# Kernel optimization log

Hardware: AMD Instinct MI355X
Metric: run time of the kernel (lower is better)

The kernel has to match this reference:

```python
import jax, jax.numpy as jnp
import numpy as np

B, S, D_IN, D_OUT, H = 2, 2048, 1024, 1024, 16
HD = D_OUT // H  # 64


def setup_inputs() -> dict:
    key = jax.random.key(0)
    ks = jax.random.split(key, 6)
    s = 0.02
    return {
        "x": jax.random.normal(ks[0], (B, S, D_IN), dtype=jnp.float32),
        "W_q": jax.random.normal(ks[1], (D_IN, D_OUT), dtype=jnp.float32) * s,
        "W_k": jax.random.normal(ks[2], (D_IN, D_OUT), dtype=jnp.float32) * s,
        "W_v": jax.random.normal(ks[3], (D_IN, D_OUT), dtype=jnp.float32) * s,
        "W_o": jax.random.normal(ks[4], (D_OUT, D_OUT), dtype=jnp.float32) * s,
        "b_o": jax.random.normal(ks[5], (D_OUT,), dtype=jnp.float32) * s,
    }


def reference(x, W_q, W_k, W_v, W_o, b_o):
    b, n, _ = x.shape
    # project and split heads: [b, h, n, hd]
    q = (x @ W_q).reshape(b, n, H, HD).transpose(0, 2, 1, 3)
    k = (x @ W_k).reshape(b, n, H, HD).transpose(0, 2, 1, 3)
    v = (x @ W_v).reshape(b, n, H, HD).transpose(0, 2, 1, 3)
    scores = jnp.einsum("bhqd,bhkd->bhqk", q, k) / jnp.sqrt(jnp.float32(HD))
    causal = jnp.tril(jnp.ones((n, n), dtype=bool))
    scores = jnp.where(causal, scores, -jnp.inf)
    attn = jax.nn.softmax(scores, axis=-1)  # dropout p=0.0 -> identity
    ctx = jnp.einsum("bhqk,bhkd->bhqd", attn, v)
    ctx = ctx.transpose(0, 2, 1, 3).reshape(b, n, D_OUT)
    return ctx @ W_o + b_o
```

## Files before the change

### kernel.cpp

```cpp
#include <hip/hip_runtime.h>

#define B_    2
#define S_    2048
#define DIN   1024
#define DOUT  1024
#define H_    16
#define HD_   64
#define M_    (B_ * S_)

typedef __bf16 bf16x8 __attribute__((ext_vector_type(8)));
typedef float  f32x4  __attribute__((ext_vector_type(4)));

__device__ __forceinline__ f32x4 MFMA(bf16x8 a, bf16x8 b, f32x4 c) {
    return __builtin_amdgcn_mfma_f32_16x16x32_bf16(a, b, c, 0, 0, 0);
}

__device__ __forceinline__ unsigned short f2b(float f) {
    union { float f; unsigned int u; } v; v.f = f;
    unsigned int u = v.u;
    return (unsigned short)((u + 0x7fffu + ((u >> 16) & 1u)) >> 16);
}

__device__ __forceinline__ unsigned pack2(float a, float b) {
    union { __bf16 h[2]; unsigned u; } cv;
    cv.h[0] = (__bf16)a; cv.h[1] = (__bf16)b;
    return cv.u;
}

#define GLDS(gp, lp) __builtin_amdgcn_global_load_lds( \
    (const __attribute__((address_space(1))) void*)(gp), \
    (__attribute__((address_space(3))) void*)(lp), 16, 0, 0)

#define QSCALE 0.1803368801111204f

__global__ __launch_bounds__(256) void k_cvt_all(const float* __restrict__ x,
                                                 const float* __restrict__ Wq,
                                                 const float* __restrict__ Wk,
                                                 const float* __restrict__ Wv,
                                                 const float* __restrict__ Wo,
                                                 unsigned short* __restrict__ xb,
                                                 unsigned short* __restrict__ WqkvT,
                                                 unsigned short* __restrict__ WoT) {
    __shared__ float tile[32][33];
    int bid = blockIdx.x;
    if (bid < 4096) {
        int i = (bid * 256 + threadIdx.x) * 4;
        float4 v = *reinterpret_cast<const float4*>(x + i);
        ushort4 o;
        o.x = f2b(v.x); o.y = f2b(v.y); o.z = f2b(v.z); o.w = f2b(v.w);
        *reinterpret_cast<ushort4*>(xb + i) = o;
        return;
    }
    int wb = bid - 4096;
    int w = wb >> 10;
    int t = wb & 1023;
    const float* src = (w == 0) ? Wq : (w == 1) ? Wk : (w == 2) ? Wv : Wo;
    unsigned short* dst = (w < 3) ? WqkvT + (size_t)w * 1024 * DIN : WoT;
    int n0 = (t & 31) * 32, k0 = (t >> 5) * 32;
    int tx = threadIdx.x & 31, ty = threadIdx.x >> 5;
    for (int i = 0; i < 4; i++)
        tile[ty + i * 8][tx] = src[(size_t)(k0 + ty + i * 8) * DOUT + n0 + tx];
    __syncthreads();
    for (int i = 0; i < 4; i++)
        dst[(size_t)(n0 + ty + i * 8) * DIN + k0 + tx] = f2b(tile[tx][ty + i * 8]);
}

__global__ __launch_bounds__(256) void k_trV(const unsigned short* __restrict__ V,
                                             unsigned short* __restrict__ Vt) {
    __shared__ unsigned short tile[64][72];
    int st = blockIdx.x, bh = blockIdx.y;
    int b = bh >> 4, h = bh & 15;
    int t = threadIdx.x;
    int r = t >> 2, c = (t & 3) << 4;
    const unsigned short* src = V + (size_t)(b * S_ + st * 64 + r) * DOUT + h * HD_ + c;
    *reinterpret_cast<int4*>(&tile[r][c])     = *reinterpret_cast<const int4*>(src);
    *reinterpret_cast<int4*>(&tile[r][c + 8]) = *reinterpret_cast<const int4*>(src + 8);
    __syncthreads();
    unsigned short o[16];
    for (int j = 0; j < 16; j++) o[j] = tile[c + j][r];
    unsigned short* dst = Vt + (size_t)(bh * 64 + r) * S_ + st * 64 + c;
    *reinterpret_cast<int4*>(dst)     = *reinterpret_cast<int4*>(&o[0]);
    *reinterpret_cast<int4*>(dst + 8) = *reinterpret_cast<int4*>(&o[8]);
}

template <int OUT_MODE>
__global__ __launch_bounds__(256) void k_gemm(const unsigned short* __restrict__ A,
                                              const unsigned short* __restrict__ Bt,
                                              unsigned short* __restrict__ Cq,
                                              unsigned short* __restrict__ Ck,
                                              unsigned short* __restrict__ Cv,
                                              float* __restrict__ Cf,
                                              const float* __restrict__ bias,
                                              int M, int N, int K, int nbx) {
    __shared__ __align__(16) unsigned short As[128 * 64];
    __shared__ __align__(16) unsigned short Bs[128 * 64];

    int nwg = gridDim.x;
    int chunkw = nwg >> 3;
    int bid = blockIdx.x;
    int nid = (bid & 7) * chunkw + (bid >> 3);
    int by = nid / nbx, bx = nid - by * nbx;
    int m0 = by * 128, n0 = bx * 128;

    int tid = threadIdx.x;
    int wid = tid >> 6, lane = tid & 63;
    int wm = wid >> 1, wn = wid & 1;
    int lr = lane & 15, lg = lane >> 4;

    f32x4 acc[4][4] = {};

    int srow = lane >> 3;
    int scol = ((lane & 7) ^ srow) * 8;
    int rsw  = lr & 7;

    for (int k0 = 0; k0 < K; k0 += 64) {
#pragma unroll
        for (int c = 0; c < 4; c++) {
            int chunk = wid * 4 + c;
            int row = chunk * 8 + srow;
            GLDS(A  + (size_t)(m0 + row) * K + k0 + scol, (char*)As + chunk * 1024);
            GLDS(Bt + (size_t)(n0 + row) * K + k0 + scol, (char*)Bs + chunk * 1024);
        }
        __syncthreads();

#pragma unroll
        for (int kk = 0; kk < 2; kk++) {
            bf16x8 af[4], bf[4];
#pragma unroll
            for (int mi = 0; mi < 4; mi++)
                af[mi] = *reinterpret_cast<const bf16x8*>(
                    &As[(wm * 64 + mi * 16 + lr) * 64 + (((kk * 4 + lg) ^ rsw) * 8)]);
#pragma unroll
            for (int ni = 0; ni < 4; ni++)
                bf[ni] = *reinterpret_cast<const bf16x8*>(
                    &Bs[(wn * 64 + ni * 16 + lr) * 64 + (((kk * 4 + lg) ^ rsw) * 8)]);
#pragma unroll
            for (int mi = 0; mi < 4; mi++)
#pragma unroll
                for (int ni = 0; ni < 4; ni++)
                    acc[mi][ni] = MFMA(af[mi], bf[ni], acc[mi][ni]);
        }
        __syncthreads();
    }

    for (int mi = 0; mi < 4; mi++)
        for (int ni = 0; ni < 4; ni++)
            for (int i = 0; i < 4; i++) {
                int row = m0 + wm * 64 + mi * 16 + lg * 4 + i;
                int col = n0 + wn * 64 + ni * 16 + lr;
                float v = acc[mi][ni][i];
                if (OUT_MODE == 2) {
                    Cf[(size_t)row * N + col] = v + bias[col];
                } else {
                    if (col < 1024)       Cq[(size_t)row * 1024 + col] = f2b(v * QSCALE);
                    else if (col < 2048)  Ck[(size_t)row * 1024 + (col - 1024)] = f2b(v);
                    else                  Cv[(size_t)row * 1024 + (col - 2048)] = f2b(v);
                }
            }
}

__global__ __launch_bounds__(512, 4) void k_attn(const unsigned short* __restrict__ Q,
                                                 const unsigned short* __restrict__ Kg,
                                                 const unsigned short* __restrict__ Vt,
                                                 unsigned short* __restrict__ ctx) {
    int p = blockIdx.x;
    int bh = blockIdx.y;
    int b = bh >> 4, h = bh & 15;
    int tid = threadIdx.x, wid = tid >> 6, lane = tid & 63;
    int lr = lane & 15, lg = lane >> 4;
    int qtB = 31 - p;
    int qt = (wid < 4) ? qtB : p;
    int q0 = qt * 64 + (wid & 3) * 16;

    __shared__ __align__(16) unsigned short Ks[2][64 * 64];
    __shared__ __align__(16) unsigned short Vs[2][64 * 64];
    __shared__ __align__(16) unsigned p_lds32[8][16 * 32];
    unsigned* pl32 = p_lds32[wid];

    const unsigned short* Qp = Q  + (size_t)b * S_ * DOUT + (size_t)h * HD_;
    const unsigned short* Kp = Kg + (size_t)b * S_ * DOUT + (size_t)h * HD_;
    const unsigned short* Vp = Vt + (size_t)(b * H_ + h) * HD_ * S_;

    bf16x8 qf0 = *reinterpret_cast<const bf16x8*>(&Qp[(size_t)(q0 + lr) * DOUT + lg * 8]);
    bf16x8 qf1 = *reinterpret_cast<const bf16x8*>(&Qp[(size_t)(q0 + lr) * DOUT + 32 + lg * 8]);
    asm volatile("" : "+v"(qf0), "+v"(qf1));

    int srow = lane >> 3;
    int scol = ((lane & 7) ^ srow) * 8;

#define STAGE_KV(buf, t)                                                           \
    {                                                                              \
        int kv0_ = (t) * 64;                                                       \
        int krow = wid * 8 + srow;                                                 \
        GLDS(Kp + (size_t)(kv0_ + krow) * DOUT + scol,                             \
             (char*)&Ks[buf][0] + wid * 1024);                                     \
        GLDS(Vp + (size_t)krow * S_ + kv0_ + scol,                                 \
             (char*)&Vs[buf][0] + wid * 1024);                                     \
    }

    STAGE_KV(0, 0)

    f32x4 o[4] = {};
    float l = 0.f;

    int ntile = qtB + 1;
    int rxor = (lr & 7) << 4;
    int qg = q0 + lr;

    for (int t = 0; t < ntile; t++) {
        int cur = t & 1;
        if (t + 1 < ntile) {
            STAGE_KV(cur ^ 1, t + 1)
            asm volatile("s_waitcnt vmcnt(2)" ::: "memory");
        } else {
            asm volatile("s_waitcnt vmcnt(0)" ::: "memory");
        }
        __builtin_amdgcn_s_barrier();

        if (t <= qt) {
            const unsigned short* Kt = Ks[cur];
            const unsigned short* Vl = Vs[cur];
            int kv0 = t * 64;

            f32x4 s[4] = {};
            __builtin_amdgcn_s_setprio(1);
#pragma unroll
            for (int nf = 0; nf < 4; nf++)
#pragma unroll
                for (int kk = 0; kk < 2; kk++) {
                    bf16x8 kf = *reinterpret_cast<const bf16x8*>(
                        &Kt[(nf * 16 + lr) * 64 + (((kk * 64 + lg * 16) ^ rxor) >> 1)]);
                    s[nf] = MFMA(kf, kk ? qf1 : qf0, s[nf]);
                }
            __builtin_amdgcn_s_setprio(0);

            if (t == qt) {
#pragma unroll
                for (int nf = 0; nf < 4; nf++)
#pragma unroll
                    for (int i = 0; i < 4; i++)
                        if (kv0 + nf * 16 + lg * 4 + i > qg) s[nf][i] = -2000.0f;
            }

            f32x4 acc = {};
#pragma unroll
            for (int nf = 0; nf < 4; nf++) {
                f32x4 pv;
#pragma unroll
                for (int i = 0; i < 4; i++) pv[i] = exp2f(s[nf][i]);
                acc += pv;
                unsigned w0 = pack2(pv[0], pv[1]);
                unsigned w1 = pack2(pv[2], pv[3]);
                int unit = (nf * 2 + (lg >> 1)) ^ (lr & 7);
                uint2 wd; wd.x = w0; wd.y = w1;
                *reinterpret_cast<uint2*>(&pl32[lr * 32 + unit * 4 + (lg & 1) * 2]) = wd;
            }
            l += (acc[0] + acc[1]) + (acc[2] + acc[3]);

            bf16x8 pf[2];
#pragma unroll
            for (int kvb = 0; kvb < 2; kvb++)
                pf[kvb] = *reinterpret_cast<const bf16x8*>(
                    &pl32[lr * 32 + (((kvb * 4 + lg) ^ (lr & 7)) * 4)]);

            __builtin_amdgcn_s_setprio(1);
#pragma unroll
            for (int nd = 0; nd < 4; nd++)
#pragma unroll
                for (int kk = 0; kk < 2; kk++) {
                    bf16x8 vf = *reinterpret_cast<const bf16x8*>(
                        &Vl[(nd * 16 + lr) * 64 + (((kk * 64 + lg * 16) ^ rxor) >> 1)]);
                    o[nd] = MFMA(pf[kk], vf, o[nd]);
                }
            __builtin_amdgcn_s_setprio(0);
        }

        __builtin_amdgcn_s_barrier();
    }

    l += __shfl_xor(l, 16, 64);
    l += __shfl_xor(l, 32, 64);

#pragma unroll
    for (int i = 0; i < 4; i++) {
        float li = __shfl(l, lg * 4 + i, 16);
        float r = __builtin_amdgcn_rcpf(li);
#pragma unroll
        for (int nd = 0; nd < 4; nd++)
            ((__bf16*)ctx)[((size_t)b * S_ + q0 + lg * 4 + i) * DOUT + h * HD_ + nd * 16 + lr] =
                (__bf16)(o[nd][i] * r);
    }
#undef STAGE_KV
}

extern "C" void kernel_launch(void* const* d_in, const int* in_sizes, int n_in,
                              void* d_out, int out_size, void* d_ws, size_t ws_size,
                              hipStream_t stream) {
    const float* x  = (const float*)d_in[0];
    const float* Wq = (const float*)d_in[1];
    const float* Wk = (const float*)d_in[2];
    const float* Wv = (const float*)d_in[3];
    const float* Wo = (const float*)d_in[4];
    const float* bo = (const float*)d_in[5];
    float* out = (float*)d_out;
    char* ws = (char*)d_ws;
    const size_t MB = 1u << 20;

    unsigned short* xb    = (unsigned short*)(ws);
    unsigned short* Vtb   = (unsigned short*)(ws);
    unsigned short* WqkvT = (unsigned short*)(ws + 8 * MB);
    unsigned short* WoT   = (unsigned short*)(ws + 14 * MB);
    unsigned short* Qb    = (unsigned short*)(ws + 16 * MB);
    unsigned short* Kb    = (unsigned short*)(ws + 24 * MB);
    unsigned short* Vb    = (unsigned short*)(ws + 32 * MB);
    unsigned short* ctx   = Vb;

    (void)in_sizes; (void)n_in; (void)out_size; (void)ws_size;

    k_cvt_all<<<8192, 256, 0, stream>>>(x, Wq, Wk, Wv, Wo, xb, WqkvT, WoT);

    k_gemm<0><<<768, 256, 0, stream>>>(xb, WqkvT, Qb, Kb, Vb, nullptr, nullptr,
                                       M_, 3072, DIN, 24);

    dim3 gt(S_ / 64, B_ * H_);
    k_trV<<<gt, 256, 0, stream>>>(Vb, Vtb);

    dim3 ga(16, B_ * H_);
    k_attn<<<ga, 512, 0, stream>>>(Qb, Kb, Vtb, ctx);

    k_gemm<2><<<256, 256, 0, stream>>>(ctx, WoT, nullptr, nullptr, nullptr,
                                       out, bo, M_, DOUT, DOUT, 8);
}
```

Before: 120.8 us.

## Process two 16-row query slices per wave in attention, halving block size

Each attention wave now handles 32 query rows (two 16-row MFMA slices) instead of 16, so the block shrinks from 8 to 4 waves while covering the same two 64-row query tiles. Each K/V fragment read from LDS feeds two MFMAs, which halves LDS read traffic per FLOP, and each wave now issues two global-to-LDS loads per tile. The trade-off is doubled accumulator and score registers per wave and fewer waves per block for hiding latency.

After: 140.0 us. 15.9% more time.

```diff
diff --git a/kernel.cpp b/kernel.cpp
--- a/kernel.cpp
+++ b/kernel.cpp
@@ -159,7 +159,7 @@
             }
 }
 
-__global__ __launch_bounds__(512, 4) void k_attn(const unsigned short* __restrict__ Q,
+__global__ __launch_bounds__(256, 4) void k_attn(const unsigned short* __restrict__ Q,
                                                  const unsigned short* __restrict__ Kg,
                                                  const unsigned short* __restrict__ Vt,
                                                  unsigned short* __restrict__ ctx) {
@@ -169,21 +169,23 @@
     int tid = threadIdx.x, wid = tid >> 6, lane = tid & 63;
     int lr = lane & 15, lg = lane >> 4;
     int qtB = 31 - p;
-    int qt = (wid < 4) ? qtB : p;
-    int q0 = qt * 64 + (wid & 3) * 16;
+    int qt = (wid < 2) ? qtB : p;
+    int q0 = qt * 64 + (wid & 1) * 32;
 
     __shared__ __align__(16) unsigned short Ks[2][64 * 64];
     __shared__ __align__(16) unsigned short Vs[2][64 * 64];
-    __shared__ __align__(16) unsigned p_lds32[8][16 * 32];
+    __shared__ __align__(16) unsigned p_lds32[4][16 * 32];
     unsigned* pl32 = p_lds32[wid];
 
     const unsigned short* Qp = Q  + (size_t)b * S_ * DOUT + (size_t)h * HD_;
     const unsigned short* Kp = Kg + (size_t)b * S_ * DOUT + (size_t)h * HD_;
     const unsigned short* Vp = Vt + (size_t)(b * H_ + h) * HD_ * S_;
 
-    bf16x8 qf0 = *reinterpret_cast<const bf16x8*>(&Qp[(size_t)(q0 + lr) * DOUT + lg * 8]);
-    bf16x8 qf1 = *reinterpret_cast<const bf16x8*>(&Qp[(size_t)(q0 + lr) * DOUT + 32 + lg * 8]);
-    asm volatile("" : "+v"(qf0), "+v"(qf1));
+    bf16x8 qf0a = *reinterpret_cast<const bf16x8*>(&Qp[(size_t)(q0 + lr) * DOUT + lg * 8]);
+    bf16x8 qf0b = *reinterpret_cast<const bf16x8*>(&Qp[(size_t)(q0 + lr) * DOUT + 32 + lg * 8]);
+    bf16x8 qf1a = *reinterpret_cast<const bf16x8*>(&Qp[(size_t)(q0 + 16 + lr) * DOUT + lg * 8]);
+    bf16x8 qf1b = *reinterpret_cast<const bf16x8*>(&Qp[(size_t)(q0 + 16 + lr) * DOUT + 32 + lg * 8]);
+    asm volatile("" : "+v"(qf0a), "+v"(qf0b), "+v"(qf1a), "+v"(qf1b));
 
     int srow = lane >> 3;
     int scol = ((lane & 7) ^ srow) * 8;
@@ -191,27 +193,30 @@
 #define STAGE_KV(buf, t)                                                           \
     {                                                                              \
         int kv0_ = (t) * 64;                                                       \
-        int krow = wid * 8 + srow;                                                 \
-        GLDS(Kp + (size_t)(kv0_ + krow) * DOUT + scol,                             \
-             (char*)&Ks[buf][0] + wid * 1024);                                     \
-        GLDS(Vp + (size_t)krow * S_ + kv0_ + scol,                                 \
-             (char*)&Vs[buf][0] + wid * 1024);                                     \
+        for (int cc = 0; cc < 2; cc++) {                                           \
+            int ch = wid * 2 + cc;                                                 \
+            int krow = ch * 8 + srow;                                              \
+            GLDS(Kp + (size_t)(kv0_ + krow) * DOUT + scol,                         \
+                 (char*)&Ks[buf][0] + ch * 1024);                                  \
+            GLDS(Vp + (size_t)krow * S_ + kv0_ + scol,                             \
+                 (char*)&Vs[buf][0] + ch * 1024);                                  \
+        }                                                                          \
     }
 
     STAGE_KV(0, 0)
 
-    f32x4 o[4] = {};
-    float l = 0.f;
+    f32x4 o0[4] = {}, o1[4] = {};
+    float l0 = 0.f, l1 = 0.f;
 
     int ntile = qtB + 1;
     int rxor = (lr & 7) << 4;
-    int qg = q0 + lr;
+    int qg0 = q0 + lr, qg1 = q0 + 16 + lr;
 
     for (int t = 0; t < ntile; t++) {
         int cur = t & 1;
         if (t + 1 < ntile) {
             STAGE_KV(cur ^ 1, t + 1)
-            asm volatile("s_waitcnt vmcnt(2)" ::: "memory");
+            asm volatile("s_waitcnt vmcnt(4)" ::: "memory");
         } else {
             asm volatile("s_waitcnt vmcnt(0)" ::: "memory");
         }
@@ -222,7 +227,7 @@
             const unsigned short* Vl = Vs[cur];
             int kv0 = t * 64;
 
-            f32x4 s[4] = {};
+            f32x4 s0[4] = {}, s1[4] = {};
             __builtin_amdgcn_s_setprio(1);
 #pragma unroll
             for (int nf = 0; nf < 4; nf++)
@@ -230,7 +235,8 @@
                 for (int kk = 0; kk < 2; kk++) {
                     bf16x8 kf = *reinterpret_cast<const bf16x8*>(
                         &Kt[(nf * 16 + lr) * 64 + (((kk * 64 + lg * 16) ^ rxor) >> 1)]);
-                    s[nf] = MFMA(kf, kk ? qf1 : qf0, s[nf]);
+                    s0[nf] = MFMA(kf, kk ? qf0b : qf0a, s0[nf]);
+                    s1[nf] = MFMA(kf, kk ? qf1b : qf1a, s1[nf]);
                 }
             __builtin_amdgcn_s_setprio(0);
 
@@ -238,30 +244,50 @@
 #pragma unroll
                 for (int nf = 0; nf < 4; nf++)
 #pragma unroll
-                    for (int i = 0; i < 4; i++)
-                        if (kv0 + nf * 16 + lg * 4 + i > qg) s[nf][i] = -2000.0f;
+                    for (int i = 0; i < 4; i++) {
+                        int kv = kv0 + nf * 16 + lg * 4 + i;
+                        if (kv > qg0) s0[nf][i] = -2000.0f;
+                        if (kv > qg1) s1[nf][i] = -2000.0f;
+                    }
             }
 
-            f32x4 acc = {};
-#pragma unroll
-            for (int nf = 0; nf < 4; nf++) {
-                f32x4 pv;
-#pragma unroll
-                for (int i = 0; i < 4; i++) pv[i] = exp2f(s[nf][i]);
-                acc += pv;
-                unsigned w0 = pack2(pv[0], pv[1]);
-                unsigned w1 = pack2(pv[2], pv[3]);
-                int unit = (nf * 2 + (lg >> 1)) ^ (lr & 7);
-                uint2 wd; wd.x = w0; wd.y = w1;
-                *reinterpret_cast<uint2*>(&pl32[lr * 32 + unit * 4 + (lg & 1) * 2]) = wd;
+            bf16x8 pf0[2], pf1[2];
+            {
+                f32x4 acc = {};
+#pragma unroll
+                for (int nf = 0; nf < 4; nf++) {
+                    f32x4 pv;
+#pragma unroll
+                    for (int i = 0; i < 4; i++) pv[i] = exp2f(s0[nf][i]);
+                    acc += pv;
+                    int unit = (nf * 2 + (lg >> 1)) ^ (lr & 7);
+                    uint2 wd; wd.x = pack2(pv[0], pv[1]); wd.y = pack2(pv[2], pv[3]);
+                    *reinterpret_cast<uint2*>(&pl32[lr * 32 + unit * 4 + (lg & 1) * 2]) = wd;
+                }
+                l0 += (acc[0] + acc[1]) + (acc[2] + acc[3]);
+#pragma unroll
+                for (int kvb = 0; kvb < 2; kvb++)
+                    pf0[kvb] = *reinterpret_cast<const bf16x8*>(
+                        &pl32[lr * 32 + (((kvb * 4 + lg) ^ (lr & 7)) * 4)]);
             }
-            l += (acc[0] + acc[1]) + (acc[2] + acc[3]);
-
-            bf16x8 pf[2];
-#pragma unroll
-            for (int kvb = 0; kvb < 2; kvb++)
-                pf[kvb] = *reinterpret_cast<const bf16x8*>(
-                    &pl32[lr * 32 + (((kvb * 4 + lg) ^ (lr & 7)) * 4)]);
+            {
+                f32x4 acc = {};
+#pragma unroll
+                for (int nf = 0; nf < 4; nf++) {
+                    f32x4 pv;
+#pragma unroll
+                    for (int i = 0; i < 4; i++) pv[i] = exp2f(s1[nf][i]);
+                    acc += pv;
+                    int unit = (nf * 2 + (lg >> 1)) ^ (lr & 7);
+                    uint2 wd; wd.x = pack2(pv[0], pv[1]); wd.y = pack2(pv[2], pv[3]);
+                    *reinterpret_cast<uint2*>(&pl32[lr * 32 + unit * 4 + (lg & 1) * 2]) = wd;
+                }
+                l1 += (acc[0] + acc[1]) + (acc[2] + acc[3]);
+#pragma unroll
+                for (int kvb = 0; kvb < 2; kvb++)
+                    pf1[kvb] = *reinterpret_cast<const bf16x8*>(
+                        &pl32[lr * 32 + (((kvb * 4 + lg) ^ (lr & 7)) * 4)]);
+            }
 
             __builtin_amdgcn_s_setprio(1);
 #pragma unroll
@@ -270,7 +296,8 @@
                 for (int kk = 0; kk < 2; kk++) {
                     bf16x8 vf = *reinterpret_cast<const bf16x8*>(
                         &Vl[(nd * 16 + lr) * 64 + (((kk * 64 + lg * 16) ^ rxor) >> 1)]);
-                    o[nd] = MFMA(pf[kk], vf, o[nd]);
+                    o0[nd] = MFMA(pf0[kk], vf, o0[nd]);
+                    o1[nd] = MFMA(pf1[kk], vf, o1[nd]);
                 }
             __builtin_amdgcn_s_setprio(0);
         }
@@ -278,17 +305,24 @@
         __builtin_amdgcn_s_barrier();
     }
 
-    l += __shfl_xor(l, 16, 64);
-    l += __shfl_xor(l, 32, 64);
+    l0 += __shfl_xor(l0, 16, 64);
+    l0 += __shfl_xor(l0, 32, 64);
+    l1 += __shfl_xor(l1, 16, 64);
+    l1 += __shfl_xor(l1, 32, 64);
 
 #pragma unroll
     for (int i = 0; i < 4; i++) {
-        float li = __shfl(l, lg * 4 + i, 16);
-        float r = __builtin_amdgcn_rcpf(li);
-#pragma unroll
-        for (int nd = 0; nd < 4; nd++)
+        float li0 = __shfl(l0, lg * 4 + i, 16);
+        float li1 = __shfl(l1, lg * 4 + i, 16);
+        float r0 = __builtin_amdgcn_rcpf(li0);
+        float r1 = __builtin_amdgcn_rcpf(li1);
+#pragma unroll
+        for (int nd = 0; nd < 4; nd++) {
             ((__bf16*)ctx)[((size_t)b * S_ + q0 + lg * 4 + i) * DOUT + h * HD_ + nd * 16 + lr] =
-                (__bf16)(o[nd][i] * r);
+                (__bf16)(o0[nd][i] * r0);
+            ((__bf16*)ctx)[((size_t)b * S_ + q0 + 16 + lg * 4 + i) * DOUT + h * HD_ + nd * 16 + lr] =
+                (__bf16)(o1[nd][i] * r1);
+        }
     }
 #undef STAGE_KV
 }
@@ -326,7 +360,7 @@
     k_trV<<<gt, 256, 0, stream>>>(Vb, Vtb);
 
     dim3 ga(16, B_ * H_);
-    k_attn<<<ga, 512, 0, stream>>>(Qb, Kb, Vtb, ctx);
+    k_attn<<<ga, 256, 0, stream>>>(Qb, Kb, Vtb, ctx);
 
     k_gemm<2><<<256, 256, 0, stream>>>(ctx, WoT, nullptr, nullptr, nullptr,
                                        out, bo, M_, DOUT, DOUT, 8);
```

## Split long causal query tile across wave groups and shrink output GEMM tile

Applied to the files above, without the earlier changes.

The attention kernel previously had one wave group process the long query tile while the other sat idle after its short tile. Now the second group finishes its short tile, then takes the remaining KV tiles of the long tile, and the two partial outputs and row sums are merged through LDS at the end. Each group gets its own double-buffered K/V staging. Separately, the output projection GEMM is templated to a 64-row M tile with twice as many blocks, to give better occupancy on a grid that was smaller than the CU count. The cost is more LDS per attention block, an extra reduction step, and lower per-block data reuse in the GEMM.

New measurement: 112.8 us. -6.6%, faster.

```diff
diff --git a/kernel.cpp b/kernel.cpp
--- a/kernel.cpp
+++ b/kernel.cpp
@@ -83,7 +83,7 @@
     *reinterpret_cast<int4*>(dst + 8) = *reinterpret_cast<int4*>(&o[8]);
 }
 
-template <int OUT_MODE>
+template <int OUT_MODE, int BM>
 __global__ __launch_bounds__(256) void k_gemm(const unsigned short* __restrict__ A,
                                               const unsigned short* __restrict__ Bt,
                                               unsigned short* __restrict__ Cq,
@@ -92,7 +92,8 @@
                                               float* __restrict__ Cf,
                                               const float* __restrict__ bias,
                                               int M, int N, int K, int nbx) {
-    __shared__ __align__(16) unsigned short As[128 * 64];
+    constexpr int MI = BM / 32;
+    __shared__ __align__(16) unsigned short As[BM * 64];
     __shared__ __align__(16) unsigned short Bs[128 * 64];
 
     int nwg = gridDim.x;
@@ -100,14 +101,14 @@
     int bid = blockIdx.x;
     int nid = (bid & 7) * chunkw + (bid >> 3);
     int by = nid / nbx, bx = nid - by * nbx;
-    int m0 = by * 128, n0 = bx * 128;
+    int m0 = by * BM, n0 = bx * 128;
 
     int tid = threadIdx.x;
     int wid = tid >> 6, lane = tid & 63;
     int wm = wid >> 1, wn = wid & 1;
     int lr = lane & 15, lg = lane >> 4;
 
-    f32x4 acc[4][4] = {};
+    f32x4 acc[MI][4] = {};
 
     int srow = lane >> 3;
     int scol = ((lane & 7) ^ srow) * 8;
@@ -115,27 +116,32 @@
 
     for (int k0 = 0; k0 < K; k0 += 64) {
 #pragma unroll
+        for (int c = 0; c < MI; c++) {
+            int chunk = wid * MI + c;
+            int row = chunk * 8 + srow;
+            GLDS(A + (size_t)(m0 + row) * K + k0 + scol, (char*)As + chunk * 1024);
+        }
+#pragma unroll
         for (int c = 0; c < 4; c++) {
             int chunk = wid * 4 + c;
             int row = chunk * 8 + srow;
-            GLDS(A  + (size_t)(m0 + row) * K + k0 + scol, (char*)As + chunk * 1024);
             GLDS(Bt + (size_t)(n0 + row) * K + k0 + scol, (char*)Bs + chunk * 1024);
         }
         __syncthreads();
 
 #pragma unroll
         for (int kk = 0; kk < 2; kk++) {
-            bf16x8 af[4], bf[4];
-#pragma unroll
-            for (int mi = 0; mi < 4; mi++)
+            bf16x8 af[MI], bf[4];
+#pragma unroll
+            for (int mi = 0; mi < MI; mi++)
                 af[mi] = *reinterpret_cast<const bf16x8*>(
-                    &As[(wm * 64 + mi * 16 + lr) * 64 + (((kk * 4 + lg) ^ rsw) * 8)]);
+                    &As[(wm * (BM / 2) + mi * 16 + lr) * 64 + (((kk * 4 + lg) ^ rsw) * 8)]);
 #pragma unroll
             for (int ni = 0; ni < 4; ni++)
                 bf[ni] = *reinterpret_cast<const bf16x8*>(
                     &Bs[(wn * 64 + ni * 16 + lr) * 64 + (((kk * 4 + lg) ^ rsw) * 8)]);
 #pragma unroll
-            for (int mi = 0; mi < 4; mi++)
+            for (int mi = 0; mi < MI; mi++)
 #pragma unroll
                 for (int ni = 0; ni < 4; ni++)
                     acc[mi][ni] = MFMA(af[mi], bf[ni], acc[mi][ni]);
@@ -143,10 +149,10 @@
         __syncthreads();
     }
 
-    for (int mi = 0; mi < 4; mi++)
+    for (int mi = 0; mi < MI; mi++)
         for (int ni = 0; ni < 4; ni++)
             for (int i = 0; i < 4; i++) {
-                int row = m0 + wm * 64 + mi * 16 + lg * 4 + i;
+                int row = m0 + wm * (BM / 2) + mi * 16 + lg * 4 + i;
                 int col = n0 + wn * 64 + ni * 16 + lr;
                 float v = acc[mi][ni][i];
                 if (OUT_MODE == 2) {
@@ -159,6 +165,64 @@
             }
 }
 
+__device__ __forceinline__ void attn_unit(const unsigned short* __restrict__ Kt,
+                                          const unsigned short* __restrict__ Vl,
+                                          unsigned* __restrict__ pl32,
+                                          bf16x8 qf0, bf16x8 qf1,
+                                          f32x4 (&o)[4], float& l,
+                                          int qg, int kv0, bool diag,
+                                          int lr, int lg, int rxor) {
+    f32x4 s[4] = {};
+    __builtin_amdgcn_s_setprio(1);
+#pragma unroll
+    for (int nf = 0; nf < 4; nf++)
+#pragma unroll
+        for (int kk = 0; kk < 2; kk++) {
+            bf16x8 kf = *reinterpret_cast<const bf16x8*>(
+                &Kt[(nf * 16 + lr) * 64 + (((kk * 64 + lg * 16) ^ rxor) >> 1)]);
+            s[nf] = MFMA(kf, kk ? qf1 : qf0, s[nf]);
+        }
+    __builtin_amdgcn_s_setprio(0);
+
+    if (diag) {
+#pragma unroll
+        for (int nf = 0; nf < 4; nf++)
+#pragma unroll
+            for (int i = 0; i < 4; i++)
+                if (kv0 + nf * 16 + lg * 4 + i > qg) s[nf][i] = -2000.0f;
+    }
+
+    f32x4 acc = {};
+#pragma unroll
+    for (int nf = 0; nf < 4; nf++) {
+        f32x4 pv;
+#pragma unroll
+        for (int i = 0; i < 4; i++) pv[i] = exp2f(s[nf][i]);
+        acc += pv;
+        int unit = (nf * 2 + (lg >> 1)) ^ (lr & 7);
+        uint2 wd; wd.x = pack2(pv[0], pv[1]); wd.y = pack2(pv[2], pv[3]);
+        *reinterpret_cast<uint2*>(&pl32[lr * 32 + unit * 4 + (lg & 1) * 2]) = wd;
+    }
+    l += (acc[0] + acc[1]) + (acc[2] + acc[3]);
+
+    bf16x8 pf[2];
+#pragma unroll
+    for (int kvb = 0; kvb < 2; kvb++)
+        pf[kvb] = *reinterpret_cast<const bf16x8*>(
+            &pl32[lr * 32 + (((kvb * 4 + lg) ^ (lr & 7)) * 4)]);
+
+    __builtin_amdgcn_s_setprio(1);
+#pragma unroll
+    for (int nd = 0; nd < 4; nd++)
+#pragma unroll
+        for (int kk = 0; kk < 2; kk++) {
+            bf16x8 vf = *reinterpret_cast<const bf16x8*>(
+                &Vl[(nd * 16 + lr) * 64 + (((kk * 64 + lg * 16) ^ rxor) >> 1)]);
+            o[nd] = MFMA(pf[kk], vf, o[nd]);
+        }
+    __builtin_amdgcn_s_setprio(0);
+}
+
 __global__ __launch_bounds__(512, 4) void k_attn(const unsigned short* __restrict__ Q,
                                                  const unsigned short* __restrict__ Kg,
                                                  const unsigned short* __restrict__ Vt,
@@ -168,12 +232,13 @@
     int b = bh >> 4, h = bh & 15;
     int tid = threadIdx.x, wid = tid >> 6, lane = tid & 63;
     int lr = lane & 15, lg = lane >> 4;
+    int g = wid >> 2, wi = wid & 3;
     int qtB = 31 - p;
-    int qt = (wid < 4) ? qtB : p;
-    int q0 = qt * 64 + (wid & 3) * 16;
-
-    __shared__ __align__(16) unsigned short Ks[2][64 * 64];
-    __shared__ __align__(16) unsigned short Vs[2][64 * 64];
+
+    __shared__ __align__(16) unsigned short Ks1[2][64 * 64];
+    __shared__ __align__(16) unsigned short Vs1[2][64 * 64];
+    __shared__ __align__(16) unsigned short Ks2[2][64 * 64];
+    __shared__ __align__(16) unsigned short Vs2[2][64 * 64];
     __shared__ __align__(16) unsigned p_lds32[8][16 * 32];
     unsigned* pl32 = p_lds32[wid];
 
@@ -181,116 +246,124 @@
     const unsigned short* Kp = Kg + (size_t)b * S_ * DOUT + (size_t)h * HD_;
     const unsigned short* Vp = Vt + (size_t)(b * H_ + h) * HD_ * S_;
 
-    bf16x8 qf0 = *reinterpret_cast<const bf16x8*>(&Qp[(size_t)(q0 + lr) * DOUT + lg * 8]);
-    bf16x8 qf1 = *reinterpret_cast<const bf16x8*>(&Qp[(size_t)(q0 + lr) * DOUT + 32 + lg * 8]);
-    asm volatile("" : "+v"(qf0), "+v"(qf1));
+    int q0B = qtB * 64 + wi * 16;
+    int q0A = p * 64 + wi * 16;
+
+    bf16x8 qB0 = *reinterpret_cast<const bf16x8*>(&Qp[(size_t)(q0B + lr) * DOUT + lg * 8]);
+    bf16x8 qB1 = *reinterpret_cast<const bf16x8*>(&Qp[(size_t)(q0B + lr) * DOUT + 32 + lg * 8]);
+    bf16x8 qA0 = {}, qA1 = {};
+    if (g == 1) {
+        qA0 = *reinterpret_cast<const bf16x8*>(&Qp[(size_t)(q0A + lr) * DOUT + lg * 8]);
+        qA1 = *reinterpret_cast<const bf16x8*>(&Qp[(size_t)(q0A + lr) * DOUT + 32 + lg * 8]);
+    }
+    asm volatile("" : "+v"(qB0), "+v"(qB1));
 
     int srow = lane >> 3;
     int scol = ((lane & 7) ^ srow) * 8;
 
-#define STAGE_KV(buf, t)                                                           \
+#define STAGE(KsX, VsX, buf, t)                                                    \
     {                                                                              \
         int kv0_ = (t) * 64;                                                       \
-        int krow = wid * 8 + srow;                                                 \
-        GLDS(Kp + (size_t)(kv0_ + krow) * DOUT + scol,                             \
-             (char*)&Ks[buf][0] + wid * 1024);                                     \
-        GLDS(Vp + (size_t)krow * S_ + kv0_ + scol,                                 \
-             (char*)&Vs[buf][0] + wid * 1024);                                     \
-    }
-
-    STAGE_KV(0, 0)
-
-    f32x4 o[4] = {};
-    float l = 0.f;
-
-    int ntile = qtB + 1;
+        for (int cc = 0; cc < 2; cc++) {                                           \
+            int ch = wi * 2 + cc;                                                  \
+            int krow = ch * 8 + srow;                                              \
+            GLDS(Kp + (size_t)(kv0_ + krow) * DOUT + scol,                         \
+                 (char*)&KsX[buf][0] + ch * 1024);                                 \
+            GLDS(Vp + (size_t)krow * S_ + kv0_ + scol,                             \
+                 (char*)&VsX[buf][0] + ch * 1024);                                 \
+        }                                                                          \
+    }
+
+    if (g == 0) STAGE(Ks1, Vs1, 0, 0)
+    else        STAGE(Ks2, Vs2, 0, 0)
+
+    f32x4 oB[4] = {}, oA[4] = {};
+    float lB = 0.f, lA = 0.f;
     int rxor = (lr & 7) << 4;
-    int qg = q0 + lr;
-
-    for (int t = 0; t < ntile; t++) {
-        int cur = t & 1;
-        if (t + 1 < ntile) {
-            STAGE_KV(cur ^ 1, t + 1)
-            asm volatile("s_waitcnt vmcnt(2)" ::: "memory");
+    int qgB = q0B + lr, qgA = q0A + lr;
+
+    for (int u = 0; u <= 16; u++) {
+        if (g == 0) {
+            if (u < 15) {
+                STAGE(Ks1, Vs1, (u + 1) & 1, u + 1)
+                asm volatile("s_waitcnt vmcnt(4)" ::: "memory");
+            } else {
+                asm volatile("s_waitcnt vmcnt(0)" ::: "memory");
+            }
         } else {
-            asm volatile("s_waitcnt vmcnt(0)" ::: "memory");
+            if (u < 16) {
+                int nt = (u + 1 <= p) ? (u + 1) : (u + 16 - p);
+                STAGE(Ks2, Vs2, (u + 1) & 1, nt)
+                asm volatile("s_waitcnt vmcnt(4)" ::: "memory");
+            } else {
+                asm volatile("s_waitcnt vmcnt(0)" ::: "memory");
+            }
         }
         __builtin_amdgcn_s_barrier();
 
-        if (t <= qt) {
-            const unsigned short* Kt = Ks[cur];
-            const unsigned short* Vl = Vs[cur];
-            int kv0 = t * 64;
-
-            f32x4 s[4] = {};
-            __builtin_amdgcn_s_setprio(1);
-#pragma unroll
-            for (int nf = 0; nf < 4; nf++)
-#pragma unroll
-                for (int kk = 0; kk < 2; kk++) {
-                    bf16x8 kf = *reinterpret_cast<const bf16x8*>(
-                        &Kt[(nf * 16 + lr) * 64 + (((kk * 64 + lg * 16) ^ rxor) >> 1)]);
-                    s[nf] = MFMA(kf, kk ? qf1 : qf0, s[nf]);
-                }
-            __builtin_amdgcn_s_setprio(0);
-
-            if (t == qt) {
-#pragma unroll
-                for (int nf = 0; nf < 4; nf++)
-#pragma unroll
-                    for (int i = 0; i < 4; i++)
-                        if (kv0 + nf * 16 + lg * 4 + i > qg) s[nf][i] = -2000.0f;
+        if (g == 0) {
+            if (u <= 15)
+                attn_unit(Ks1[u & 1], Vs1[u & 1], pl32, qB0, qB1, oB, lB,
+                          qgB, u * 64, false, lr, lg, rxor);
+        } else {
+            if (u <= p)
+                attn_unit(Ks2[u & 1], Vs2[u & 1], pl32, qA0, qA1, oA, lA,
+                          qgA, u * 64, u == p, lr, lg, rxor);
+            else {
+                int t = u + 15 - p;
+                attn_unit(Ks2[u & 1], Vs2[u & 1], pl32, qB0, qB1, oB, lB,
+                          qgB, t * 64, t == qtB, lr, lg, rxor);
             }
-
-            f32x4 acc = {};
-#pragma unroll
-            for (int nf = 0; nf < 4; nf++) {
-                f32x4 pv;
-#pragma unroll
-                for (int i = 0; i < 4; i++) pv[i] = exp2f(s[nf][i]);
-                acc += pv;
-                unsigned w0 = pack2(pv[0], pv[1]);
-                unsigned w1 = pack2(pv[2], pv[3]);
-                int unit = (nf * 2 + (lg >> 1)) ^ (lr & 7);
-                uint2 wd; wd.x = w0; wd.y = w1;
-                *reinterpret_cast<uint2*>(&pl32[lr * 32 + unit * 4 + (lg & 1) * 2]) = wd;
-            }
-            l += (acc[0] + acc[1]) + (acc[2] + acc[3]);
-
-            bf16x8 pf[2];
-#pragma unroll
-            for (int kvb = 0; kvb < 2; kvb++)
-                pf[kvb] = *reinterpret_cast<const bf16x8*>(
-                    &pl32[lr * 32 + (((kvb * 4 + lg) ^ (lr & 7)) * 4)]);
-
-            __builtin_amdgcn_s_setprio(1);
+        }
+        __builtin_amdgcn_s_barrier();
+    }
+
+    float* mO = (float*)&Ks1[0][0];
+    float* mL = (float*)&Vs1[0][0];
+
+    if (g == 1) {
+        lA += __shfl_xor(lA, 16, 64);
+        lA += __shfl_xor(lA, 32, 64);
+#pragma unroll
+        for (int i = 0; i < 4; i++) {
+            float li = __shfl(lA, lg * 4 + i, 16);
+            float r = __builtin_amdgcn_rcpf(li);
 #pragma unroll
             for (int nd = 0; nd < 4; nd++)
-#pragma unroll
-                for (int kk = 0; kk < 2; kk++) {
-                    bf16x8 vf = *reinterpret_cast<const bf16x8*>(
-                        &Vl[(nd * 16 + lr) * 64 + (((kk * 64 + lg * 16) ^ rxor) >> 1)]);
-                    o[nd] = MFMA(pf[kk], vf, o[nd]);
-                }
-            __builtin_amdgcn_s_setprio(0);
-        }
-
-        __builtin_amdgcn_s_barrier();
-    }
-
-    l += __shfl_xor(l, 16, 64);
-    l += __shfl_xor(l, 32, 64);
-
-#pragma unroll
-    for (int i = 0; i < 4; i++) {
-        float li = __shfl(l, lg * 4 + i, 16);
-        float r = __builtin_amdgcn_rcpf(li);
+                ((__bf16*)ctx)[((size_t)b * S_ + q0A + lg * 4 + i) * DOUT + h * HD_ + nd * 16 + lr] =
+                    (__bf16)(oA[nd][i] * r);
+        }
+        int base = (wi * 64 + lane) * 16;
 #pragma unroll
         for (int nd = 0; nd < 4; nd++)
-            ((__bf16*)ctx)[((size_t)b * S_ + q0 + lg * 4 + i) * DOUT + h * HD_ + nd * 16 + lr] =
-                (__bf16)(o[nd][i] * r);
-    }
-#undef STAGE_KV
+#pragma unroll
+            for (int i = 0; i < 4; i++)
+                mO[base + nd * 4 + i] = oB[nd][i];
+        mL[wi * 64 + lane] = lB;
+    }
+    asm volatile("s_waitcnt lgkmcnt(0)" ::: "memory");
+    __builtin_amdgcn_s_barrier();
+    if (g == 0) {
+        int base = (wi * 64 + lane) * 16;
+#pragma unroll
+        for (int nd = 0; nd < 4; nd++)
+#pragma unroll
+            for (int i = 0; i < 4; i++)
+                oB[nd][i] += mO[base + nd * 4 + i];
+        lB += mL[wi * 64 + lane];
+        lB += __shfl_xor(lB, 16, 64);
+        lB += __shfl_xor(lB, 32, 64);
+#pragma unroll
+        for (int i = 0; i < 4; i++) {
+            float li = __shfl(lB, lg * 4 + i, 16);
+            float r = __builtin_amdgcn_rcpf(li);
+#pragma unroll
+            for (int nd = 0; nd < 4; nd++)
+                ((__bf16*)ctx)[((size_t)b * S_ + q0B + lg * 4 + i) * DOUT + h * HD_ + nd * 16 + lr] =
+                    (__bf16)(oB[nd][i] * r);
+        }
+    }
+#undef STAGE
 }
 
 extern "C" void kernel_launch(void* const* d_in, const int* in_sizes, int n_in,
@@ -319,8 +392,8 @@
 
     k_cvt_all<<<8192, 256, 0, stream>>>(x, Wq, Wk, Wv, Wo, xb, WqkvT, WoT);
 
-    k_gemm<0><<<768, 256, 0, stream>>>(xb, WqkvT, Qb, Kb, Vb, nullptr, nullptr,
-                                       M_, 3072, DIN, 24);
+    k_gemm<0, 128><<<768, 256, 0, stream>>>(xb, WqkvT, Qb, Kb, Vb, nullptr, nullptr,
+                                            M_, 3072, DIN, 24);
 
     dim3 gt(S_ / 64, B_ * H_);
     k_trV<<<gt, 256, 0, stream>>>(Vb, Vtb);
@@ -328,6 +401,6 @@
     dim3 ga(16, B_ * H_);
     k_attn<<<ga, 512, 0, stream>>>(Qb, Kb, Vtb, ctx);
 
-    k_gemm<2><<<256, 256, 0, stream>>>(ctx, WoT, nullptr, nullptr, nullptr,
-                                       out, bo, M_, DOUT, DOUT, 8);
-}
+    k_gemm<2, 64><<<512, 256, 0, stream>>>(ctx, WoT, nullptr, nullptr, nullptr,
+                                           out, bo, M_, DOUT, DOUT, 8);
+}
```
